# Kernel optimization log

Measured on AMD Instinct MI355X. Metric: run time of the kernel, lower is better.

Reference implementation:

```python
import jax, jax.numpy as jnp
import numpy as np


def setup_inputs() -> dict:
    key = jax.random.key(0)
    ks_ = jax.random.split(key, 12)
    B, Q, K, D, d = 8, 4096, 4096, 256, 64
    s = 1.0 / np.sqrt(D)
    inp = {
        "qs": jax.random.normal(ks_[0], (B, Q, D), jnp.float32),
        "ks": jax.random.normal(ks_[1], (B, K, D), jnp.float32),
        "vs": jax.random.normal(ks_[2], (B, K, D), jnp.float32),
        "valid_lens": jax.random.randint(ks_[3], (B,), 1, K + 1, jnp.int32),
        "Wq": jax.random.normal(ks_[4], (D, d), jnp.float32) * s,
        "bq": jnp.zeros((d,), jnp.float32),
        "Wk": jax.random.normal(ks_[5], (D, d), jnp.float32) * s,
        "bk": jnp.zeros((d,), jnp.float32),
        "Wv": jax.random.normal(ks_[6], (D, d), jnp.float32) * s,
        "bv": jnp.zeros((d,), jnp.float32),
        "Wo": jax.random.normal(ks_[7], (d, d), jnp.float32) * (1.0 / np.sqrt(d)),
        "bo": jnp.zeros((d,), jnp.float32),
    }
    return inp


def reference(qs, ks, vs, valid_lens, Wq, bq, Wk, bk, Wv, bv, Wo, bo):
    # Linear projections (default MLP([64]) heads)
    q = qs @ Wq + bq          # [B, Q, d]
    k = ks @ Wk + bk          # [B, K, d]
    v = vs @ Wv + bv          # [B, K, d]

    # RBF kernel scores: exp(-||q_i - k_j||^2 / sqrt(d)).
    # Expand ||q-k||^2 = ||q||^2 + ||k||^2 - 2 q.k to avoid the [B,Q,K,d]
    # pairwise-difference tensor the original materializes.
    q2 = jnp.sum(q * q, axis=-1)                         # [B, Q]
    k2 = jnp.sum(k * k, axis=-1)                         # [B, K]
    qk = jnp.einsum("bqd,bkd->bqk", q, k)                # [B, Q, K]
    d_sq = jnp.maximum(q2[:, :, None] + k2[:, None, :] - 2.0 * qk, 0.0)
    attn = jnp.exp(-d_sq / jnp.sqrt(jnp.asarray(k.shape[-1], q.dtype)))

    # Mask invalid keys (fill=0.0), then row-normalize.
    key_ids = jnp.arange(k.shape[1])                     # [K]
    mask = key_ids[None, None, :] < valid_lens[:, None, None]
    attn = jnp.where(mask, attn, 0.0)
    attn = attn / jnp.sum(attn, axis=-1, keepdims=True)

    ctx = attn @ v                                       # [B, Q, d]
    out = ctx @ Wo + bo                                  # [B, Q, d]
    return out, attn
```

## Files before the change

### kernel.cpp

```cpp
#include <hip/hip_runtime.h>
#include <hip/hip_bf16.h>


typedef _Float16 HALF;
typedef HALF half8 __attribute__((ext_vector_type(8)));
typedef __fp16 fp16x2 __attribute__((ext_vector_type(2)));
typedef float f32x4 __attribute__((ext_vector_type(4)));

#define MFMA16(a, b, c) __builtin_amdgcn_mfma_f32_16x16x32_f16((a), (b), (c), 0, 0, 0)

union Cv4 { HALF h[4]; uint2 u; };
union Cv8 { HALF h[8]; uint4 u; };
union PK8 { fp16x2 p2[4]; half8 v; };

__global__ __launch_bounds__(256) void k_prep(const float* __restrict__ Wq,
                                              const float* __restrict__ Wk,
                                              const float* __restrict__ Wv,
                                              const float* __restrict__ Wo,
                                              HALF* __restrict__ wt,
                                              HALF* __restrict__ wto) {
    int gid = blockIdx.x * 256 + threadIdx.x;
    if (gid < 49152) {
        int t = gid >> 14;
        int rem = gid & 16383;
        int n = rem >> 8, k = rem & 255;
        const float* W = (t == 0) ? Wq : ((t == 1) ? Wk : Wv);
        wt[gid] = (HALF)W[k * 64 + n];
    } else {
        int rem = gid - 49152;
        int n = rem >> 6, k = rem & 63;
        wto[rem] = (HALF)Wo[k * 64 + n];
    }
}

__global__ __launch_bounds__(256, 2) void k_proj(const float* __restrict__ qs,
                                                 const float* __restrict__ ks,
                                                 const float* __restrict__ vs,
                                                 const float* __restrict__ bq,
                                                 const float* __restrict__ bk,
                                                 const float* __restrict__ bv,
                                                 const HALF* __restrict__ wt,
                                                 HALF* __restrict__ qh,
                                                 HALF* __restrict__ kh,
                                                 HALF* __restrict__ vth,
                                                 float* __restrict__ kcw) {
    int bid = blockIdx.x;
    int t = bid >> 9;
    int rem = bid & 511;
    int b = rem & 7, rt = rem >> 3;
    int m0 = rt * 64;
    const float* X    = (t == 0) ? qs : ((t == 1) ? ks : vs);
    const float* bias = (t == 0) ? bq : ((t == 1) ? bk : bv);

    __shared__ char smem[67584];
    HALF (*sW)[264]  = (HALF(*)[264])smem;
    HALF (*sX)[264]  = (HALF(*)[264])(smem + 33792);
    float (*sOut)[68] = (float(*)[68])(smem + 33792);

    int tid = threadIdx.x;
    int w = tid >> 6, lane = tid & 63, ln = lane & 15, quad = lane >> 4;

    const HALF* wsrc = wt + t * 16384;
#pragma unroll
    for (int s = 0; s < 8; ++s) {
        int flat = (s * 256 + tid) * 8;
        int r = flat >> 8, c = flat & 255;
        *(uint4*)&sW[r][c] = *(const uint4*)(wsrc + flat);
    }
    const float* xbase = X + ((size_t)(b * 4096 + m0)) * 256;
#pragma unroll
    for (int s = 0; s < 16; ++s) {
        int flat = (s * 256 + tid) * 4;
        int r = flat >> 8, c = flat & 255;
        float4 xv = *(const float4*)(xbase + flat);
        Cv4 cv; cv.h[0] = (HALF)xv.x; cv.h[1] = (HALF)xv.y;
        cv.h[2] = (HALF)xv.z; cv.h[3] = (HALF)xv.w;
        *(uint2*)&sX[r][c] = cv.u;
    }
    __syncthreads();

    f32x4 zero4 = {0.f, 0.f, 0.f, 0.f};
    f32x4 acc[4] = {zero4, zero4, zero4, zero4};
#pragma unroll
    for (int kb = 0; kb < 8; ++kb) {
        half8 a = *(half8*)&sX[w * 16 + ln][kb * 32 + quad * 8];
#pragma unroll
        for (int t4 = 0; t4 < 4; ++t4) {
            half8 bf = *(half8*)&sW[t4 * 16 + ln][kb * 32 + quad * 8];
            acc[t4] = MFMA16(a, bf, acc[t4]);
        }
    }
    __syncthreads();

    float bias_v[4];
#pragma unroll
    for (int t4 = 0; t4 < 4; ++t4) bias_v[t4] = bias[t4 * 16 + ln];

    float rsq[4] = {0.f, 0.f, 0.f, 0.f};
#pragma unroll
    for (int t4 = 0; t4 < 4; ++t4) {
#pragma unroll
        for (int r = 0; r < 4; ++r) {
            float v = acc[t4][r] + bias_v[t4];
            rsq[r] += v * v;
            sOut[w * 16 + quad * 4 + r][t4 * 16 + ln] = v;
        }
    }
    if (t == 1) {
#pragma unroll
        for (int r = 0; r < 4; ++r) {
            float v = rsq[r];
#pragma unroll
            for (int off = 1; off < 16; off <<= 1) v += __shfl_xor(v, off);
            if (ln == 0) kcw[b * 4096 + m0 + w * 16 + quad * 4 + r] = -0.125f * v;
        }
    }
    __syncthreads();

    if (t < 2) {
        HALF* dst = ((t == 0) ? qh : kh) + ((size_t)(b * 4096 + m0)) * 64;
#pragma unroll
        for (int s = 0; s < 4; ++s) {
            int flat = (s * 256 + tid) * 4;
            int r = flat >> 6, c = flat & 63;
            float4 v = *(float4*)&sOut[r][c];
            Cv4 cv; cv.h[0] = (HALF)v.x; cv.h[1] = (HALF)v.y;
            cv.h[2] = (HALF)v.z; cv.h[3] = (HALF)v.w;
            *(uint2*)(dst + flat) = cv.u;
        }
    } else {
        HALF* dst = vth + (size_t)b * 64 * 4096 + m0;
#pragma unroll
        for (int s = 0; s < 2; ++s) {
            int dv = s * 32 + (tid >> 3);
            int kc = (tid & 7) * 8;
            Cv8 cv;
#pragma unroll
            for (int i = 0; i < 8; ++i) cv.h[i] = (HALF)sOut[kc + i][dv];
            *(uint4*)(dst + (size_t)dv * 4096 + kc) = cv.u;
        }
    }
}

__global__ __launch_bounds__(256, 4) void k_attn(const HALF* __restrict__ qh,
                                                 const HALF* __restrict__ kh,
                                                 const HALF* __restrict__ vth,
                                                 const float* __restrict__ kcw,
                                                 const int* __restrict__ vlen,
                                                 const HALF* __restrict__ wto,
                                                 const float* __restrict__ bo,
                                                 float* __restrict__ attn_out,
                                                 float* __restrict__ out) {
    int bid = blockIdx.x;
    int qt = bid >> 3;
    int b = (bid + qt) & 7;
    int m0 = qt * 64;
    int tid = threadIdx.x;
    int w = tid >> 6, lane = tid & 63, ln = lane & 15, quad = lane >> 4;
    int valid = vlen[b];

    __shared__ char smem[36352];
    HALF (*sK)[72]  = (HALF(*)[72])smem;
    HALF (*sVt)[72] = (HALF(*)[72])(smem + 9216);
    float (*sS)[68] = (float(*)[68])(smem + 18432);
    HALF (*sQ)[72]  = (HALF(*)[72])(smem + 18432);
    HALF (*sWo)[72] = (HALF(*)[72])smem;
    float* sKC = (float*)(smem + 35840);
    float* sRS = (float*)(smem + 36096);

    const HALF* qbase = qh + ((size_t)(b * 4096 + m0)) * 64;
    { int f0 = tid * 8;         *(uint4*)&sQ[f0 >> 6][f0 & 63] = *(const uint4*)(qbase + f0);
      int f1 = (256 + tid) * 8; *(uint4*)&sQ[f1 >> 6][f1 & 63] = *(const uint4*)(qbase + f1); }
    __syncthreads();
    half8 qa0, qa1;
    { int row = w * 16 + ln, k0 = quad * 8;
      qa0 = *(half8*)&sQ[row][k0];
      qa1 = *(half8*)&sQ[row][32 + k0]; }
    __syncthreads();

    int nvt = (valid + 63) >> 6;
    const HALF* kbb = kh + (size_t)b * 4096 * 64;
    const HALF* vtb = vth + (size_t)b * 64 * 4096;
    const float* kcb = kcw + b * 4096;
    const float NEG_INF = -__builtin_inff();

    uint4 kr0, kr1; float kcr = 0.f;
    kr0 = *(const uint4*)(kbb + tid * 8);
    kr1 = *(const uint4*)(kbb + (256 + tid) * 8);
    if (tid < 64) kcr = kcb[tid];

    float rs[4] = {0.f, 0.f, 0.f, 0.f};
    for (int nt = 0; nt < nvt; ++nt) {
        int n0 = nt * 64;
        { int f0 = tid * 8;         *(uint4*)&sK[f0 >> 6][f0 & 63] = kr0;
          int f1 = (256 + tid) * 8; *(uint4*)&sK[f1 >> 6][f1 & 63] = kr1; }
        if (tid < 64) sKC[tid] = (n0 + tid < valid) ? kcr : NEG_INF;
        __syncthreads();
        if (nt + 1 < nvt) {
            const HALF* src = kbb + (size_t)(nt + 1) * 4096;
            kr0 = *(const uint4*)(src + tid * 8);
            kr1 = *(const uint4*)(src + (256 + tid) * 8);
            if (tid < 64) kcr = kcb[n0 + 64 + tid];
        }
#pragma unroll
        for (int t4 = 0; t4 < 4; ++t4) {
            f32x4 acc = {0.f, 0.f, 0.f, 0.f};
            half8 b0 = *(half8*)&sK[t4 * 16 + ln][quad * 8];
            half8 b1 = *(half8*)&sK[t4 * 16 + ln][32 + quad * 8];
            acc = MFMA16(qa0, b0, acc);
            acc = MFMA16(qa1, b1, acc);
            float kcv = sKC[t4 * 16 + ln];
#pragma unroll
            for (int r = 0; r < 4; ++r)
                rs[r] += __expf(fmaf(acc[r], 0.25f, kcv));
        }
        __syncthreads();
    }

#pragma unroll
    for (int r = 0; r < 4; ++r) {
        float v = rs[r];
#pragma unroll
        for (int off = 1; off < 16; off <<= 1) v += __shfl_xor(v, off);
        rs[r] = v;
    }
    if (ln == 0) {
#pragma unroll
        for (int r = 0; r < 4; ++r) sRS[w * 16 + quad * 4 + r] = rs[r];
    }
    __syncthreads();
    if (tid < 64) sRS[tid] = 1.0f / sRS[tid];
    __syncthreads();
    float inv_r[4];
#pragma unroll
    for (int r = 0; r < 4; ++r) inv_r[r] = sRS[w * 16 + quad * 4 + r];

    f32x4 cz = {0.f, 0.f, 0.f, 0.f};
    f32x4 cacc[4] = {cz, cz, cz, cz};
    float* attn_base = attn_out + ((size_t)(b * 4096 + m0)) * 4096;

    uint4 vr0, vr1;
    kr0 = *(const uint4*)(kbb + tid * 8);
    kr1 = *(const uint4*)(kbb + (256 + tid) * 8);
    { int f0 = tid * 8, f1 = (256 + tid) * 8;
      vr0 = *(const uint4*)(vtb + (size_t)(f0 >> 6) * 4096 + (f0 & 63));
      vr1 = *(const uint4*)(vtb + (size_t)(f1 >> 6) * 4096 + (f1 & 63)); }
    if (tid < 64) kcr = kcb[tid];

    for (int nt = 0; nt < nvt; ++nt) {
        int n0 = nt * 64;
        { int f0 = tid * 8, f1 = (256 + tid) * 8;
          *(uint4*)&sK[f0 >> 6][f0 & 63] = kr0;
          *(uint4*)&sK[f1 >> 6][f1 & 63] = kr1;
          *(uint4*)&sVt[f0 >> 6][f0 & 63] = vr0;
          *(uint4*)&sVt[f1 >> 6][f1 & 63] = vr1; }
        if (tid < 64) sKC[tid] = (n0 + tid < valid) ? kcr : NEG_INF;
        __syncthreads();
        if (nt + 1 < nvt) {
            const HALF* ksrc = kbb + (size_t)(nt + 1) * 4096;
            int f0 = tid * 8, f1 = (256 + tid) * 8;
            kr0 = *(const uint4*)(ksrc + f0);
            kr1 = *(const uint4*)(ksrc + f1);
            vr0 = *(const uint4*)(vtb + (size_t)(f0 >> 6) * 4096 + n0 + 64 + (f0 & 63));
            vr1 = *(const uint4*)(vtb + (size_t)(f1 >> 6) * 4096 + n0 + 64 + (f1 & 63));
            if (tid < 64) kcr = kcb[n0 + 64 + tid];
        }
#pragma unroll
        for (int t4 = 0; t4 < 4; ++t4) {
            f32x4 acc = {0.f, 0.f, 0.f, 0.f};
            half8 b0 = *(half8*)&sK[t4 * 16 + ln][quad * 8];
            half8 b1 = *(half8*)&sK[t4 * 16 + ln][32 + quad * 8];
            acc = MFMA16(qa0, b0, acc);
            acc = MFMA16(qa1, b1, acc);
            int col = t4 * 16 + ln;
            float kcv = sKC[col];
#pragma unroll
            for (int r = 0; r < 4; ++r) {
                int row = w * 16 + quad * 4 + r;
                sS[row][col] = __expf(fmaf(acc[r], 0.25f, kcv)) * inv_r[r];
            }
        }
        __syncthreads();
#pragma unroll
        for (int s = 0; s < 4; ++s) {
            int row = s * 16 + (tid >> 4);
            int col = (tid & 15) * 4;
            *(float4*)(attn_base + (size_t)row * 4096 + n0 + col) = *(float4*)&sS[row][col];
        }
#pragma unroll
        for (int ks2 = 0; ks2 < 2; ++ks2) {
            const float* sp = &sS[w * 16 + ln][ks2 * 32 + quad * 8];
            float4 f0 = *(float4*)sp;
            float4 f1 = *((float4*)sp + 1);
            PK8 pk;
            pk.p2[0] = __builtin_amdgcn_cvt_pkrtz(f0.x, f0.y);
            pk.p2[1] = __builtin_amdgcn_cvt_pkrtz(f0.z, f0.w);
            pk.p2[2] = __builtin_amdgcn_cvt_pkrtz(f1.x, f1.y);
            pk.p2[3] = __builtin_amdgcn_cvt_pkrtz(f1.z, f1.w);
            half8 pa = pk.v;
#pragma unroll
            for (int t4 = 0; t4 < 4; ++t4) {
                half8 vb = *(half8*)&sVt[t4 * 16 + ln][ks2 * 32 + quad * 8];
                cacc[t4] = MFMA16(pa, vb, cacc[t4]);
            }
        }
        __syncthreads();
    }

    float4 z4 = {0.f, 0.f, 0.f, 0.f};
    for (int nt = nvt; nt < 64; ++nt) {
        int n0 = nt * 64;
#pragma unroll
        for (int s = 0; s < 4; ++s) {
            int row = s * 16 + (tid >> 4);
            int col = (tid & 15) * 4;
            *(float4*)(attn_base + (size_t)row * 4096 + n0 + col) = z4;
        }
    }

#pragma unroll
    for (int t4 = 0; t4 < 4; ++t4) {
#pragma unroll
        for (int r = 0; r < 4; ++r)
            sS[w * 16 + quad * 4 + r][t4 * 16 + ln] = cacc[t4][r];
    }
    { int f0 = tid * 8;         *(uint4*)&sWo[f0 >> 6][f0 & 63] = *(const uint4*)(wto + f0);
      int f1 = (256 + tid) * 8; *(uint4*)&sWo[f1 >> 6][f1 & 63] = *(const uint4*)(wto + f1); }
    __syncthreads();

    f32x4 oacc[4] = {cz, cz, cz, cz};
#pragma unroll
    for (int ks2 = 0; ks2 < 2; ++ks2) {
        const float* sp = &sS[w * 16 + ln][ks2 * 32 + quad * 8];
        float4 f0 = *(float4*)sp;
        float4 f1 = *((float4*)sp + 1);
        PK8 pk;
        pk.p2[0] = __builtin_amdgcn_cvt_pkrtz(f0.x, f0.y);
        pk.p2[1] = __builtin_amdgcn_cvt_pkrtz(f0.z, f0.w);
        pk.p2[2] = __builtin_amdgcn_cvt_pkrtz(f1.x, f1.y);
        pk.p2[3] = __builtin_amdgcn_cvt_pkrtz(f1.z, f1.w);
        half8 a = pk.v;
#pragma unroll
        for (int t4 = 0; t4 < 4; ++t4) {
            half8 bf = *(half8*)&sWo[t4 * 16 + ln][ks2 * 32 + quad * 8];
            oacc[t4] = MFMA16(a, bf, oacc[t4]);
        }
    }
    float* obase = out + ((size_t)(b * 4096 + m0)) * 64;
#pragma unroll
    for (int t4 = 0; t4 < 4; ++t4) {
        float bov = bo[t4 * 16 + ln];
#pragma unroll
        for (int r = 0; r < 4; ++r)
            obase[(size_t)(w * 16 + quad * 4 + r) * 64 + t4 * 16 + ln] = oacc[t4][r] + bov;
    }
}

extern "C" void kernel_launch(void* const* d_in, const int* in_sizes, int n_in,
                              void* d_out, int out_size, void* d_ws, size_t ws_size,
                              hipStream_t stream) {
    const float* qs = (const float*)d_in[0];
    const float* ks = (const float*)d_in[1];
    const float* vs = (const float*)d_in[2];
    const int* vlen = (const int*)d_in[3];
    const float* Wq = (const float*)d_in[4];
    const float* bq = (const float*)d_in[5];
    const float* Wk = (const float*)d_in[6];
    const float* bk = (const float*)d_in[7];
    const float* Wv = (const float*)d_in[8];
    const float* bv = (const float*)d_in[9];
    const float* Wo = (const float*)d_in[10];
    const float* bo = (const float*)d_in[11];

    float* out  = (float*)d_out;
    float* attn = out + 2097152;

    char* wsb = (char*)d_ws;
    HALF*  wt  = (HALF*)(wsb + 0);
    HALF*  wto = (HALF*)(wsb + 98304);
    HALF*  qh  = (HALF*)(wsb + 131072);
    HALF*  kh  = (HALF*)(wsb + 4325376);
    HALF*  vth = (HALF*)(wsb + 8519680);
    float* kcw = (float*)(wsb + 12713984);

    k_prep<<<208, 256, 0, stream>>>(Wq, Wk, Wv, Wo, wt, wto);
    k_proj<<<1536, 256, 0, stream>>>(qs, ks, vs, bq, bk, bv, wt, qh, kh, vth, kcw);
    k_attn<<<512, 256, 0, stream>>>(qh, kh, vth, kcw, vlen, wto, bo, attn, out);
}
```

Baseline: 689.1 us.

## Restructure attention kernel to single-wave blocks with register-resident operands and no LDS

The attention kernel now uses one 64-lane wave per 16-query block instead of four waves per 64 queries. It drops shared memory and barriers, loading K, V^T and Wo fragments straight from global memory into registers, and it computes S transposed so each lane holds contiguous attention columns for direct nontemporal float4 stores. The key mask is folded into the projection kernel by writing -inf into the key norm term, which removes the per-tile mask logic. The cost is more redundant global and L2 reads of K and V, since four times as many blocks each stream them.

```diff
diff --git a/kernel.cpp b/kernel.cpp
--- a/kernel.cpp
+++ b/kernel.cpp
@@ -4,14 +4,16 @@
 
 typedef _Float16 HALF;
 typedef HALF half8 __attribute__((ext_vector_type(8)));
+typedef HALF half4 __attribute__((ext_vector_type(4)));
 typedef __fp16 fp16x2 __attribute__((ext_vector_type(2)));
 typedef float f32x4 __attribute__((ext_vector_type(4)));
 
-#define MFMA16(a, b, c) __builtin_amdgcn_mfma_f32_16x16x32_f16((a), (b), (c), 0, 0, 0)
+#define MFMA32(a, b, c) __builtin_amdgcn_mfma_f32_16x16x32_f16((a), (b), (c), 0, 0, 0)
+#define MFMA16x16(a, b, c) __builtin_amdgcn_mfma_f32_16x16x16f16((a), (b), (c), 0, 0, 0)
 
 union Cv4 { HALF h[4]; uint2 u; };
 union Cv8 { HALF h[8]; uint4 u; };
-union PK8 { fp16x2 p2[4]; half8 v; };
+union PK4 { fp16x2 p2[2]; half4 v; };
 
 __global__ __launch_bounds__(256) void k_prep(const float* __restrict__ Wq,
                                               const float* __restrict__ Wk,
@@ -39,6 +41,7 @@
                                                  const float* __restrict__ bq,
                                                  const float* __restrict__ bk,
                                                  const float* __restrict__ bv,
+                                                 const int* __restrict__ vlen,
                                                  const HALF* __restrict__ wt,
                                                  HALF* __restrict__ qh,
                                                  HALF* __restrict__ kh,
@@ -51,6 +54,7 @@
     int m0 = rt * 64;
     const float* X    = (t == 0) ? qs : ((t == 1) ? ks : vs);
     const float* bias = (t == 0) ? bq : ((t == 1) ? bk : bv);
+    int valid = vlen[b];
 
     __shared__ char smem[67584];
     HALF (*sW)[264]  = (HALF(*)[264])smem;
@@ -87,7 +91,7 @@
 #pragma unroll
         for (int t4 = 0; t4 < 4; ++t4) {
             half8 bf = *(half8*)&sW[t4 * 16 + ln][kb * 32 + quad * 8];
-            acc[t4] = MFMA16(a, bf, acc[t4]);
+            acc[t4] = MFMA32(a, bf, acc[t4]);
         }
     }
     __syncthreads();
@@ -112,7 +116,10 @@
             float v = rsq[r];
 #pragma unroll
             for (int off = 1; off < 16; off <<= 1) v += __shfl_xor(v, off);
-            if (ln == 0) kcw[b * 4096 + m0 + w * 16 + quad * 4 + r] = -0.125f * v;
+            if (ln == 0) {
+                int kidx = m0 + w * 16 + quad * 4 + r;
+                kcw[b * 4096 + kidx] = (kidx < valid) ? -0.125f * v : -__builtin_inff();
+            }
         }
     }
     __syncthreads();
@@ -142,217 +149,162 @@
     }
 }
 
-__global__ __launch_bounds__(256, 4) void k_attn(const HALF* __restrict__ qh,
-                                                 const HALF* __restrict__ kh,
-                                                 const HALF* __restrict__ vth,
-                                                 const float* __restrict__ kcw,
-                                                 const int* __restrict__ vlen,
-                                                 const HALF* __restrict__ wto,
-                                                 const float* __restrict__ bo,
-                                                 float* __restrict__ attn_out,
-                                                 float* __restrict__ out) {
+__global__ __launch_bounds__(64, 2) void k_attn(const HALF* __restrict__ qh,
+                                                const HALF* __restrict__ kh,
+                                                const HALF* __restrict__ vth,
+                                                const float* __restrict__ kcw,
+                                                const int* __restrict__ vlen,
+                                                const HALF* __restrict__ wto,
+                                                const float* __restrict__ bo,
+                                                float* __restrict__ attn_out,
+                                                float* __restrict__ out) {
     int bid = blockIdx.x;
-    int qt = bid >> 3;
-    int b = (bid + qt) & 7;
-    int m0 = qt * 64;
-    int tid = threadIdx.x;
-    int w = tid >> 6, lane = tid & 63, ln = lane & 15, quad = lane >> 4;
+    int rg  = bid >> 3;
+    int b   = (bid & 7) ^ ((rg & 1) << 2);
+    int m0  = rg * 16;
+    int lane = threadIdx.x;
+    int ln = lane & 15, quad = lane >> 4;
     int valid = vlen[b];
-
-    __shared__ char smem[36352];
-    HALF (*sK)[72]  = (HALF(*)[72])smem;
-    HALF (*sVt)[72] = (HALF(*)[72])(smem + 9216);
-    float (*sS)[68] = (float(*)[68])(smem + 18432);
-    HALF (*sQ)[72]  = (HALF(*)[72])(smem + 18432);
-    HALF (*sWo)[72] = (HALF(*)[72])smem;
-    float* sKC = (float*)(smem + 35840);
-    float* sRS = (float*)(smem + 36096);
-
-    const HALF* qbase = qh + ((size_t)(b * 4096 + m0)) * 64;
-    { int f0 = tid * 8;         *(uint4*)&sQ[f0 >> 6][f0 & 63] = *(const uint4*)(qbase + f0);
-      int f1 = (256 + tid) * 8; *(uint4*)&sQ[f1 >> 6][f1 & 63] = *(const uint4*)(qbase + f1); }
-    __syncthreads();
-    half8 qa0, qa1;
-    { int row = w * 16 + ln, k0 = quad * 8;
-      qa0 = *(half8*)&sQ[row][k0];
-      qa1 = *(half8*)&sQ[row][32 + k0]; }
-    __syncthreads();
-
     int nvt = (valid + 63) >> 6;
-    const HALF* kbb = kh + (size_t)b * 4096 * 64;
-    const HALF* vtb = vth + (size_t)b * 64 * 4096;
+
+    const HALF*  kb  = kh  + (size_t)b * 4096 * 64;
+    const HALF*  vtb = vth + (size_t)b * 64 * 4096;
     const float* kcb = kcw + b * 4096;
-    const float NEG_INF = -__builtin_inff();
-
-    uint4 kr0, kr1; float kcr = 0.f;
-    kr0 = *(const uint4*)(kbb + tid * 8);
-    kr1 = *(const uint4*)(kbb + (256 + tid) * 8);
-    if (tid < 64) kcr = kcb[tid];
-
-    float rs[4] = {0.f, 0.f, 0.f, 0.f};
+
+    const HALF* qrow = qh + ((size_t)(b * 4096 + m0 + ln)) * 64 + quad * 8;
+    half8 qb0 = *(const half8*)qrow;
+    half8 qb1 = *(const half8*)(qrow + 32);
+
+    const HALF* kfb = kb + (size_t)ln * 64 + quad * 8;
+    f32x4 zz = {0.f, 0.f, 0.f, 0.f};
+
+    half8 ka[4][2];
+#pragma unroll
+    for (int t4 = 0; t4 < 4; ++t4) {
+        ka[t4][0] = *(const half8*)(kfb + t4 * 1024);
+        ka[t4][1] = *(const half8*)(kfb + t4 * 1024 + 32);
+    }
+    float rs = 0.f;
     for (int nt = 0; nt < nvt; ++nt) {
-        int n0 = nt * 64;
-        { int f0 = tid * 8;         *(uint4*)&sK[f0 >> 6][f0 & 63] = kr0;
-          int f1 = (256 + tid) * 8; *(uint4*)&sK[f1 >> 6][f1 & 63] = kr1; }
-        if (tid < 64) sKC[tid] = (n0 + tid < valid) ? kcr : NEG_INF;
-        __syncthreads();
-        if (nt + 1 < nvt) {
-            const HALF* src = kbb + (size_t)(nt + 1) * 4096;
-            kr0 = *(const uint4*)(src + tid * 8);
-            kr1 = *(const uint4*)(src + (256 + tid) * 8);
-            if (tid < 64) kcr = kcb[n0 + 64 + tid];
-        }
-#pragma unroll
-        for (int t4 = 0; t4 < 4; ++t4) {
-            f32x4 acc = {0.f, 0.f, 0.f, 0.f};
-            half8 b0 = *(half8*)&sK[t4 * 16 + ln][quad * 8];
-            half8 b1 = *(half8*)&sK[t4 * 16 + ln][32 + quad * 8];
-            acc = MFMA16(qa0, b0, acc);
-            acc = MFMA16(qa1, b1, acc);
-            float kcv = sKC[t4 * 16 + ln];
+        f32x4 kcv[4];
+        const float* kcp = kcb + (nt << 6) + quad * 4;
+#pragma unroll
+        for (int t4 = 0; t4 < 4; ++t4) kcv[t4] = *(const f32x4*)(kcp + t4 * 16);
+
+        f32x4 acc[4];
+#pragma unroll
+        for (int t4 = 0; t4 < 4; ++t4) {
+            acc[t4] = MFMA32(ka[t4][0], qb0, zz);
+            acc[t4] = MFMA32(ka[t4][1], qb1, acc[t4]);
+        }
+        int n1 = (nt + 1 < nvt ? nt + 1 : nt) << 6;
+        const HALF* kf = kfb + (size_t)n1 * 64;
+#pragma unroll
+        for (int t4 = 0; t4 < 4; ++t4) {
+            ka[t4][0] = *(const half8*)(kf + t4 * 1024);
+            ka[t4][1] = *(const half8*)(kf + t4 * 1024 + 32);
+        }
+#pragma unroll
+        for (int t4 = 0; t4 < 4; ++t4) {
 #pragma unroll
             for (int r = 0; r < 4; ++r)
-                rs[r] += __expf(fmaf(acc[r], 0.25f, kcv));
-        }
-        __syncthreads();
-    }
-
-#pragma unroll
-    for (int r = 0; r < 4; ++r) {
-        float v = rs[r];
-#pragma unroll
-        for (int off = 1; off < 16; off <<= 1) v += __shfl_xor(v, off);
-        rs[r] = v;
-    }
-    if (ln == 0) {
-#pragma unroll
-        for (int r = 0; r < 4; ++r) sRS[w * 16 + quad * 4 + r] = rs[r];
-    }
-    __syncthreads();
-    if (tid < 64) sRS[tid] = 1.0f / sRS[tid];
-    __syncthreads();
-    float inv_r[4];
-#pragma unroll
-    for (int r = 0; r < 4; ++r) inv_r[r] = sRS[w * 16 + quad * 4 + r];
-
-    f32x4 cz = {0.f, 0.f, 0.f, 0.f};
-    f32x4 cacc[4] = {cz, cz, cz, cz};
-    float* attn_base = attn_out + ((size_t)(b * 4096 + m0)) * 4096;
-
-    uint4 vr0, vr1;
-    kr0 = *(const uint4*)(kbb + tid * 8);
-    kr1 = *(const uint4*)(kbb + (256 + tid) * 8);
-    { int f0 = tid * 8, f1 = (256 + tid) * 8;
-      vr0 = *(const uint4*)(vtb + (size_t)(f0 >> 6) * 4096 + (f0 & 63));
-      vr1 = *(const uint4*)(vtb + (size_t)(f1 >> 6) * 4096 + (f1 & 63)); }
-    if (tid < 64) kcr = kcb[tid];
+                rs += __expf(fmaf(acc[t4][r], 0.25f, kcv[t4][r]));
+        }
+    }
+    rs += __shfl_xor(rs, 16);
+    rs += __shfl_xor(rs, 32);
+    float inv = 1.0f / rs;
+
+#pragma unroll
+    for (int t4 = 0; t4 < 4; ++t4) {
+        ka[t4][0] = *(const half8*)(kfb + t4 * 1024);
+        ka[t4][1] = *(const half8*)(kfb + t4 * 1024 + 32);
+    }
+    f32x4 cacc[4] = {zz, zz, zz, zz};
+    float* arow = attn_out + ((size_t)(b * 4096 + m0 + ln)) * 4096 + quad * 4;
+    const HALF* vfb = vtb + (size_t)ln * 4096 + quad * 4;
 
     for (int nt = 0; nt < nvt; ++nt) {
-        int n0 = nt * 64;
-        { int f0 = tid * 8, f1 = (256 + tid) * 8;
-          *(uint4*)&sK[f0 >> 6][f0 & 63] = kr0;
-          *(uint4*)&sK[f1 >> 6][f1 & 63] = kr1;
-          *(uint4*)&sVt[f0 >> 6][f0 & 63] = vr0;
-          *(uint4*)&sVt[f1 >> 6][f1 & 63] = vr1; }
-        if (tid < 64) sKC[tid] = (n0 + tid < valid) ? kcr : NEG_INF;
-        __syncthreads();
-        if (nt + 1 < nvt) {
-            const HALF* ksrc = kbb + (size_t)(nt + 1) * 4096;
-            int f0 = tid * 8, f1 = (256 + tid) * 8;
-            kr0 = *(const uint4*)(ksrc + f0);
-            kr1 = *(const uint4*)(ksrc + f1);
-            vr0 = *(const uint4*)(vtb + (size_t)(f0 >> 6) * 4096 + n0 + 64 + (f0 & 63));
-            vr1 = *(const uint4*)(vtb + (size_t)(f1 >> 6) * 4096 + n0 + 64 + (f1 & 63));
-            if (tid < 64) kcr = kcb[n0 + 64 + tid];
-        }
-#pragma unroll
-        for (int t4 = 0; t4 < 4; ++t4) {
-            f32x4 acc = {0.f, 0.f, 0.f, 0.f};
-            half8 b0 = *(half8*)&sK[t4 * 16 + ln][quad * 8];
-            half8 b1 = *(half8*)&sK[t4 * 16 + ln][32 + quad * 8];
-            acc = MFMA16(qa0, b0, acc);
-            acc = MFMA16(qa1, b1, acc);
-            int col = t4 * 16 + ln;
-            float kcv = sKC[col];
-#pragma unroll
-            for (int r = 0; r < 4; ++r) {
-                int row = w * 16 + quad * 4 + r;
-                sS[row][col] = __expf(fmaf(acc[r], 0.25f, kcv)) * inv_r[r];
-            }
-        }
-        __syncthreads();
-#pragma unroll
-        for (int s = 0; s < 4; ++s) {
-            int row = s * 16 + (tid >> 4);
-            int col = (tid & 15) * 4;
-            *(float4*)(attn_base + (size_t)row * 4096 + n0 + col) = *(float4*)&sS[row][col];
-        }
-#pragma unroll
-        for (int ks2 = 0; ks2 < 2; ++ks2) {
-            const float* sp = &sS[w * 16 + ln][ks2 * 32 + quad * 8];
-            float4 f0 = *(float4*)sp;
-            float4 f1 = *((float4*)sp + 1);
-            PK8 pk;
-            pk.p2[0] = __builtin_amdgcn_cvt_pkrtz(f0.x, f0.y);
-            pk.p2[1] = __builtin_amdgcn_cvt_pkrtz(f0.z, f0.w);
-            pk.p2[2] = __builtin_amdgcn_cvt_pkrtz(f1.x, f1.y);
-            pk.p2[3] = __builtin_amdgcn_cvt_pkrtz(f1.z, f1.w);
-            half8 pa = pk.v;
-#pragma unroll
-            for (int t4 = 0; t4 < 4; ++t4) {
-                half8 vb = *(half8*)&sVt[t4 * 16 + ln][ks2 * 32 + quad * 8];
-                cacc[t4] = MFMA16(pa, vb, cacc[t4]);
-            }
-        }
-        __syncthreads();
-    }
-
-    float4 z4 = {0.f, 0.f, 0.f, 0.f};
+        int n0 = nt << 6;
+        f32x4 kcv[4];
+        const float* kcp = kcb + n0 + quad * 4;
+#pragma unroll
+        for (int t4 = 0; t4 < 4; ++t4) kcv[t4] = *(const f32x4*)(kcp + t4 * 16);
+
+        half4 va[4][4];
+#pragma unroll
+        for (int t4dv = 0; t4dv < 4; ++t4dv)
+#pragma unroll
+            for (int t4k = 0; t4k < 4; ++t4k)
+                va[t4dv][t4k] = *(const half4*)(vfb + (size_t)t4dv * 65536 + n0 + t4k * 16);
+
+        f32x4 acc[4];
+#pragma unroll
+        for (int t4 = 0; t4 < 4; ++t4) {
+            acc[t4] = MFMA32(ka[t4][0], qb0, zz);
+            acc[t4] = MFMA32(ka[t4][1], qb1, acc[t4]);
+        }
+        int n1 = (nt + 1 < nvt ? nt + 1 : nt) << 6;
+        const HALF* kf = kfb + (size_t)n1 * 64;
+#pragma unroll
+        for (int t4 = 0; t4 < 4; ++t4) {
+            ka[t4][0] = *(const half8*)(kf + t4 * 1024);
+            ka[t4][1] = *(const half8*)(kf + t4 * 1024 + 32);
+        }
+
+        float p[4][4];
+#pragma unroll
+        for (int t4 = 0; t4 < 4; ++t4) {
+#pragma unroll
+            for (int r = 0; r < 4; ++r)
+                p[t4][r] = __expf(fmaf(acc[t4][r], 0.25f, kcv[t4][r])) * inv;
+            f32x4 st = {p[t4][0], p[t4][1], p[t4][2], p[t4][3]};
+            __builtin_nontemporal_store(st, (f32x4*)(arow + n0 + t4 * 16));
+        }
+        half4 pb[4];
+#pragma unroll
+        for (int t4 = 0; t4 < 4; ++t4) {
+            PK4 pk;
+            pk.p2[0] = __builtin_amdgcn_cvt_pkrtz(p[t4][0], p[t4][1]);
+            pk.p2[1] = __builtin_amdgcn_cvt_pkrtz(p[t4][2], p[t4][3]);
+            pb[t4] = pk.v;
+        }
+#pragma unroll
+        for (int t4dv = 0; t4dv < 4; ++t4dv)
+#pragma unroll
+            for (int t4k = 0; t4k < 4; ++t4k)
+                cacc[t4dv] = MFMA16x16(va[t4dv][t4k], pb[t4k], cacc[t4dv]);
+    }
+
     for (int nt = nvt; nt < 64; ++nt) {
-        int n0 = nt * 64;
-#pragma unroll
-        for (int s = 0; s < 4; ++s) {
-            int row = s * 16 + (tid >> 4);
-            int col = (tid & 15) * 4;
-            *(float4*)(attn_base + (size_t)row * 4096 + n0 + col) = z4;
-        }
-    }
-
+#pragma unroll
+        for (int t4 = 0; t4 < 4; ++t4)
+            __builtin_nontemporal_store(zz, (f32x4*)(arow + (nt << 6) + t4 * 16));
+    }
+
+    half4 cb[4];
 #pragma unroll
     for (int t4 = 0; t4 < 4; ++t4) {
-#pragma unroll
-        for (int r = 0; r < 4; ++r)
-            sS[w * 16 + quad * 4 + r][t4 * 16 + ln] = cacc[t4][r];
-    }
-    { int f0 = tid * 8;         *(uint4*)&sWo[f0 >> 6][f0 & 63] = *(const uint4*)(wto + f0);
-      int f1 = (256 + tid) * 8; *(uint4*)&sWo[f1 >> 6][f1 & 63] = *(const uint4*)(wto + f1); }
-    __syncthreads();
-
-    f32x4 oacc[4] = {cz, cz, cz, cz};
-#pragma unroll
-    for (int ks2 = 0; ks2 < 2; ++ks2) {
-        const float* sp = &sS[w * 16 + ln][ks2 * 32 + quad * 8];
-        float4 f0 = *(float4*)sp;
-        float4 f1 = *((float4*)sp + 1);
-        PK8 pk;
-        pk.p2[0] = __builtin_amdgcn_cvt_pkrtz(f0.x, f0.y);
-        pk.p2[1] = __builtin_amdgcn_cvt_pkrtz(f0.z, f0.w);
-        pk.p2[2] = __builtin_amdgcn_cvt_pkrtz(f1.x, f1.y);
-        pk.p2[3] = __builtin_amdgcn_cvt_pkrtz(f1.z, f1.w);
-        half8 a = pk.v;
-#pragma unroll
-        for (int t4 = 0; t4 < 4; ++t4) {
-            half8 bf = *(half8*)&sWo[t4 * 16 + ln][ks2 * 32 + quad * 8];
-            oacc[t4] = MFMA16(a, bf, oacc[t4]);
-        }
-    }
-    float* obase = out + ((size_t)(b * 4096 + m0)) * 64;
-#pragma unroll
-    for (int t4 = 0; t4 < 4; ++t4) {
-        float bov = bo[t4 * 16 + ln];
-#pragma unroll
-        for (int r = 0; r < 4; ++r)
-            obase[(size_t)(w * 16 + quad * 4 + r) * 64 + t4 * 16 + ln] = oacc[t4][r] + bov;
+        PK4 pk;
+        pk.p2[0] = __builtin_amdgcn_cvt_pkrtz(cacc[t4][0], cacc[t4][1]);
+        pk.p2[1] = __builtin_amdgcn_cvt_pkrtz(cacc[t4][2], cacc[t4][3]);
+        cb[t4] = pk.v;
+    }
+    f32x4 oacc[4] = {zz, zz, zz, zz};
+    const HALF* wfb = wto + ln * 64 + quad * 4;
+#pragma unroll
+    for (int t4o = 0; t4o < 4; ++t4o)
+#pragma unroll
+        for (int t4c = 0; t4c < 4; ++t4c) {
+            half4 wa = *(const half4*)(wfb + t4o * 1024 + t4c * 16);
+            oacc[t4o] = MFMA16x16(wa, cb[t4c], oacc[t4o]);
+        }
+    float* orow = out + ((size_t)(b * 4096 + m0 + ln)) * 64 + quad * 4;
+#pragma unroll
+    for (int t4o = 0; t4o < 4; ++t4o) {
+        f32x4 bo4 = *(const f32x4*)(bo + t4o * 16 + quad * 4);
+        f32x4 ov = oacc[t4o] + bo4;
+        *(f32x4*)(orow + t4o * 16) = ov;
     }
 }
 
@@ -384,6 +336,6 @@
     float* kcw = (float*)(wsb + 12713984);
 
     k_prep<<<208, 256, 0, stream>>>(Wq, Wk, Wv, Wo, wt, wto);
-    k_proj<<<1536, 256, 0, stream>>>(qs, ks, vs, bq, bk, bv, wt, qh, kh, vth, kcw);
-    k_attn<<<512, 256, 0, stream>>>(qh, kh, vth, kcw, vlen, wto, bo, attn, out);
+    k_proj<<<1536, 256, 0, stream>>>(qs, ks, vs, bq, bk, bv, vlen, wt, qh, kh, vth, kcw);
+    k_attn<<<2048, 64, 0, stream>>>(qh, kh, vth, kcw, vlen, wto, bo, attn, out);
 }
```

After: 947.4 us. 37.5% more time.
